# Kernel tuning notes

Measured on AMD Instinct MI355X. Metric: run time of the kernel, lower is better.

Reference implementation:

```python
import jax, jax.numpy as jnp
import numpy as np

LN_EPS = 1e-12


def setup_inputs() -> dict:
    key = jax.random.key(0)
    ks = jax.random.split(key, 5)
    b, t, n, di, do, de = 2, 3, 4096, 64, 64, 64
    return {
        "x": jax.random.normal(ks[0], (b, t, n, di), dtype=jnp.float32),
        "node_emb": jax.random.normal(ks[1], (n, de), dtype=jnp.float32),
        "time_emb": jax.random.normal(ks[2], (b, t, de), dtype=jnp.float32),
        "weights_pool": jax.random.normal(ks[3], (de, 2, di, do), dtype=jnp.float32) * 0.05,
        "bias_pool": jax.random.normal(ks[4], (de, do), dtype=jnp.float32) * 0.05,
        "ln_gamma": jnp.ones((de,), dtype=jnp.float32),
        "ln_beta": jnp.zeros((de,), dtype=jnp.float32),
    }


def reference(x, node_emb, time_emb, weights_pool, bias_pool, ln_gamma, ln_beta):
    # x: (b,t,n,di); node_emb: (n,de); time_emb: (b,t,de)
    # Dropout is identity in eval mode.
    e = node_emb[None, None, :, :] + time_emb[:, :, None, :]          # (b,t,n,de)
    mu = jnp.mean(e, axis=-1, keepdims=True)
    var = jnp.var(e, axis=-1, keepdims=True)
    e = (e - mu) * jax.lax.rsqrt(var + LN_EPS) * ln_gamma + ln_beta    # LayerNorm
    # Dynamic adjacency: softmax over source nodes
    supports2 = jax.nn.softmax(jnp.einsum("btnd,btmd->btnm", e, e), axis=-1)
    # supports1 is the identity matrix -> x_g1 == x
    x_g1 = x
    x_g2 = jnp.einsum("btnm,btmc->btnc", supports2, x)
    x_g = jnp.stack([x_g1, x_g2], axis=3)                              # (b,t,n,k=2,di)
    # Hypernetwork weights: node embeddings are identical for every t,
    # so tnd,dkio->tnkio reduces to nd,dkio->nkio (broadcast over t).
    weights = jnp.einsum("nd,dkio->nkio", node_emb, weights_pool)      # (n,2,di,do)
    bias = jnp.einsum("btd,do->bto", time_emb, bias_pool)              # (b,t,do)
    out = jnp.einsum("btnki,nkio->btno", x_g, weights) + bias[:, :, None, :]
    return out
```

## Files before the change

kernel.cpp:

```cpp
#include <hip/hip_runtime.h>


using bf16x8 = __attribute__((ext_vector_type(8))) __bf16;
using f32x4  = __attribute__((ext_vector_type(4))) float;
using f32x16 = __attribute__((ext_vector_type(16))) float;
using u32x4  = __attribute__((ext_vector_type(4))) unsigned int;

__device__ __forceinline__ unsigned short f2bf_bits(float f) {
    unsigned int u = __float_as_uint(f);
    u += 0x7fffu + ((u >> 16) & 1u);
    return (unsigned short)(u >> 16);
}

__device__ __forceinline__ unsigned int PK(float a, float b) {
    return __builtin_amdgcn_perm(__float_as_uint(b), __float_as_uint(a),
                                 0x07060302u);
}

__device__ __forceinline__ f32x4 mfma16(bf16x8 a, bf16x8 b, f32x4 c) {
    return __builtin_amdgcn_mfma_f32_16x16x32_bf16(a, b, c, 0, 0, 0);
}
__device__ __forceinline__ f32x16 mfma32(bf16x8 a, bf16x8 b, f32x16 c) {
    return __builtin_amdgcn_mfma_f32_32x32x16_bf16(a, b, c, 0, 0, 0);
}
__device__ __forceinline__ f32x16 zero16() {
    f32x16 z;
    #pragma unroll
    for (int i = 0; i < 16; ++i) z[i] = 0.f;
    return z;
}

__global__ __launch_bounds__(256) void k_prep(const float* __restrict__ x,
                                              const float* __restrict__ node_emb,
                                              const float* __restrict__ time_emb,
                                              const float* __restrict__ wp,
                                              const float* __restrict__ bias_pool,
                                              const float* __restrict__ gamma,
                                              const float* __restrict__ beta,
                                              unsigned short* __restrict__ eT,
                                              unsigned short* __restrict__ vT,
                                              unsigned short* __restrict__ ne_bf,
                                              unsigned short* __restrict__ wpB,
                                              float* __restrict__ biasw) {
    __shared__ float tile[64 * 65];
    const int b = blockIdx.x;
    const int t = threadIdx.x;
    if (b < 1536) {
        int lane = t & 63;
        int row0 = b * 16 + ((t >> 6) << 2);
        float gm = gamma[lane], bb2 = beta[lane];
        #pragma unroll
        for (int ri = 0; ri < 4; ++ri) {
            int rowf = row0 + ri;
            int bt = rowf >> 12, row = rowf & 4095;
            float v = node_emb[(row << 6) | lane] + time_emb[(bt << 6) | lane];
            float s = v, s2 = v * v;
            #pragma unroll
            for (int off = 32; off; off >>= 1) {
                s  += __shfl_xor(s,  off);
                s2 += __shfl_xor(s2, off);
            }
            float mu  = s * 0.015625f;
            float var = s2 * 0.015625f - mu * mu;
            float r   = rsqrtf(var + 1e-12f);
            float o   = (v - mu) * r * gm + bb2;
            size_t idx = (size_t)bt * 262144 + ((row >> 5) << 11)
                       + ((lane >> 4) << 9) + (((lane >> 3) & 1) << 8)
                       + ((row & 31) << 3) + (lane & 7);
            eT[idx] = f2bf_bits(o);
        }
    } else if (b < 1920) {
        int bb = b - 1536;
        int bt = bb >> 6, n0 = (bb & 63) << 6;
        const float* xr = x + ((size_t)((bt << 12) | n0) << 6);
        #pragma unroll
        for (int it = 0; it < 16; ++it) {
            int i = (it << 2) + (t >> 6);
            int d = t & 63;
            tile[i * 65 + d] = xr[(i << 6) + d];
        }
        __syncthreads();
        unsigned short* dst = vT + (size_t)bt * 262144;
        #pragma unroll
        for (int it = 0; it < 16; ++it) {
            int d = (it << 2) + (t >> 6);
            int n = t & 63;
            dst[(((n0 + n) >> 3) << 9) + (d << 3) + (n & 7)]
                = f2bf_bits(tile[n * 65 + d]);
        }
    } else if (b < 2944) {
        int idx = (b - 1920) * 256 + t;
        ne_bf[idx] = f2bf_bits(node_emb[idx]);
    } else if (b < 3072) {
        int ki = b - 2944;
        #pragma unroll
        for (int it = 0; it < 16; ++it) {
            int d = (it << 2) + (t >> 6);
            int o = t & 63;
            tile[d * 65 + o] = wp[(d << 13) + (ki << 6) + o];
        }
        __syncthreads();
        unsigned short* dst = wpB + ((size_t)ki << 12);
        #pragma unroll
        for (int it = 0; it < 2; ++it) {
            int u    = (it << 8) + t;
            int ot   = u >> 7;
            int frag = (u >> 6) & 1;
            int pos  = u & 63;
            int quad = pos >> 4, l16 = pos & 15;
            unsigned short* dp = dst + ((((ot << 1) + frag) << 9) + (pos << 3));
            #pragma unroll
            for (int j = 0; j < 8; ++j)
                dp[j] = f2bf_bits(
                    tile[((frag << 5) + (quad << 3) + j) * 65 + (ot << 4) + l16]);
        }
    } else {
        for (int idx = t; idx < 384; idx += 256) {
            int bt = idx >> 6, o = idx & 63;
            float bsum = 0.f;
            for (int d = 0; d < 64; ++d)
                bsum += time_emb[(bt << 6) + d] * bias_pool[(d << 6) + o];
            biasw[idx] = bsum;
        }
    }
}

__global__ __launch_bounds__(256, 3) void k_attn(const unsigned short* __restrict__ eT,
                                                 const unsigned short* __restrict__ vT,
                                                 float* __restrict__ P0,
                                                 float* __restrict__ P1,
                                                 float* __restrict__ L0,
                                                 float* __restrict__ L1) {
    __shared__ __align__(16) float Obuf[2][32 * 68];
    __shared__ float l_s[4][32];
    const int tid  = threadIdx.x;
    const int w    = tid >> 6;
    const int lane = tid & 63;
    const int l32  = lane & 31;
    const int h    = lane >> 5;

    const int bid   = blockIdx.x;
    const int half  = bid & 1;
    const int inner = bid >> 1;
    const int x8    = inner & 7;
    const int g     = (inner >> 3) & 31;
    const int r3    = inner >> 8;
    const int combo = x8 * 3 + r3;
    const int bt    = combo >> 2;
    const int qbase = ((((combo & 3) << 5) + g) << 5);

    const unsigned short* eb = eT + (size_t)bt * 262144;
    const unsigned short* vb = vT + (size_t)bt * 262144;
    float* Pout = half ? P1 : P0;
    float* Lout = half ? L1 : L0;

    const unsigned short* qp = eb + ((qbase >> 5) << 11) + (h << 8) + (l32 << 3);
    bf16x8 qf[4];
    #pragma unroll
    for (int c = 0; c < 4; ++c) {
        bf16x8 q = *(const bf16x8*)(qp + (c << 9));
        #pragma unroll
        for (int j = 0; j < 8; ++j) q[j] = (__bf16)((float)q[j] * 1.44269504f);
        qf[c] = q;
    }

    f32x16 O0 = zero16(), O1 = zero16();
    float lsa[4] = {0.f, 0.f, 0.f, 0.f};

    const int kstart = (half << 11) + (w << 9);
    const unsigned short* krBase = eb + ((kstart >> 5) << 11) + (h << 8) + (l32 << 3);
    const unsigned short* vrBase = vb + ((kstart >> 3) << 9) + (h << 9) + (l32 << 3);

    bf16x8 kA0, kA1, kA2, kA3, vA0, vA1, vA2, vA3;
    bf16x8 kB0, kB1, kB2, kB3, vB0, vB1, vB2, vB3;

#define LOAD_GRP(gi, K0, K1, K2, K3, V0, V1, V2, V3)                    \
    {                                                                   \
        const unsigned short* kp = krBase + ((gi) << 11);               \
        const unsigned short* vp = vrBase + ((gi) << 11);               \
        K0 = *(const bf16x8*)(kp);                                      \
        K1 = *(const bf16x8*)(kp + 512);                                \
        K2 = *(const bf16x8*)(kp + 1024);                               \
        K3 = *(const bf16x8*)(kp + 1536);                               \
        V0 = *(const bf16x8*)(vp);                                      \
        V1 = *(const bf16x8*)(vp + 256);                                \
        V2 = *(const bf16x8*)(vp + 1024);                               \
        V3 = *(const bf16x8*)(vp + 1280);                               \
    }

#define COMPUTE_GRP(K0, K1, K2, K3, V0, V1, V2, V3)                     \
    {                                                                   \
        f32x16 S = zero16();                                            \
        S = mfma32(K0, qf[0], S);                                       \
        S = mfma32(K1, qf[1], S);                                       \
        S = mfma32(K2, qf[2], S);                                       \
        S = mfma32(K3, qf[3], S);                                       \
        float p[16];                                                    \
        _Pragma("unroll")                                               \
        for (int r = 0; r < 16; ++r) p[r] = __builtin_amdgcn_exp2f(S[r]); \
        _Pragma("unroll")                                               \
        for (int r = 0; r < 4; ++r)                                     \
            lsa[r] += (p[r] + p[r + 4]) + (p[r + 8] + p[r + 12]);       \
        unsigned int Pa = PK(p[0], p[1]),   Pb = PK(p[2], p[3]);        \
        unsigned int Pc = PK(p[4], p[5]),   Pd = PK(p[6], p[7]);        \
        unsigned int Pe = PK(p[8], p[9]),   Pf = PK(p[10], p[11]);      \
        unsigned int Pg = PK(p[12], p[13]), Ph = PK(p[14], p[15]);      \
        unsigned int e0 = (unsigned int)__shfl_xor((int)(h ? Pa : Pc), 32); \
        unsigned int e1 = (unsigned int)__shfl_xor((int)(h ? Pb : Pd), 32); \
        unsigned int e2 = (unsigned int)__shfl_xor((int)(h ? Pe : Pg), 32); \
        unsigned int e3 = (unsigned int)__shfl_xor((int)(h ? Pf : Ph), 32); \
        u32x4 w0 = { h ? e0 : Pa, h ? e1 : Pb,                          \
                     h ? Pc : e0, h ? Pd : e1 };                        \
        u32x4 w1 = { h ? e2 : Pe, h ? e3 : Pf,                          \
                     h ? Pg : e2, h ? Ph : e3 };                        \
        bf16x8 pf0 = __builtin_bit_cast(bf16x8, w0);                    \
        bf16x8 pf1 = __builtin_bit_cast(bf16x8, w1);                    \
        O0 = mfma32(pf0, V0, O0);                                       \
        O1 = mfma32(pf0, V1, O1);                                       \
        O0 = mfma32(pf1, V2, O0);                                       \
        O1 = mfma32(pf1, V3, O1);                                       \
    }

    LOAD_GRP(0, kA0, kA1, kA2, kA3, vA0, vA1, vA2, vA3);
    for (int gi = 0; gi < 14; gi += 2) {
        LOAD_GRP(gi + 1, kB0, kB1, kB2, kB3, vB0, vB1, vB2, vB3);
        COMPUTE_GRP(kA0, kA1, kA2, kA3, vA0, vA1, vA2, vA3);
        LOAD_GRP(gi + 2, kA0, kA1, kA2, kA3, vA0, vA1, vA2, vA3);
        COMPUTE_GRP(kB0, kB1, kB2, kB3, vB0, vB1, vB2, vB3);
    }
    LOAD_GRP(15, kB0, kB1, kB2, kB3, vB0, vB1, vB2, vB3);
    COMPUTE_GRP(kA0, kA1, kA2, kA3, vA0, vA1, vA2, vA3);
    COMPUTE_GRP(kB0, kB1, kB2, kB3, vB0, vB1, vB2, vB3);
#undef LOAD_GRP
#undef COMPUTE_GRP

    float ls = (lsa[0] + lsa[1]) + (lsa[2] + lsa[3]);
    float lsum2 = ls + __shfl_xor(ls, 32);
    if (h == 0) l_s[w][l32] = lsum2;
    float* buf = Obuf[w & 1];
    if (w < 2) {
        #pragma unroll
        for (int r = 0; r < 16; ++r) {
            int qrow = (r & 3) + ((r >> 2) << 3) + (h << 2);
            buf[qrow * 68 + l32]      = O0[r];
            buf[qrow * 68 + 32 + l32] = O1[r];
        }
    }
    __syncthreads();
    if (w >= 2) {
        #pragma unroll
        for (int r = 0; r < 16; ++r) {
            int qrow = (r & 3) + ((r >> 2) << 3) + (h << 2);
            buf[qrow * 68 + l32]      += O0[r];
            buf[qrow * 68 + 32 + l32] += O1[r];
        }
    }
    __syncthreads();
    {
        int q  = tid >> 3;
        int d0 = (tid & 7) << 3;
        const float* b0 = Obuf[0] + q * 68 + d0;
        const float* b1 = Obuf[1] + q * 68 + d0;
        float* dst = Pout + (((size_t)(bt << 12) + qbase + q) << 6) + d0;
        #pragma unroll
        for (int i = 0; i < 8; ++i) dst[i] = b0[i] + b1[i];
        if ((tid & 7) == 0)
            Lout[(bt << 12) + qbase + q] =
                l_s[0][q] + l_s[1][q] + l_s[2][q] + l_s[3][q];
    }
}

__global__ __launch_bounds__(256, 2) void k_hyper(const float* __restrict__ x,
                                                  const float* __restrict__ P0,
                                                  const float* __restrict__ P1,
                                                  const float* __restrict__ L0,
                                                  const float* __restrict__ L1,
                                                  const unsigned short* __restrict__ ne_bf,
                                                  const unsigned short* __restrict__ wpB,
                                                  const float* __restrict__ bias_ws,
                                                  float* __restrict__ out) {
    __shared__ float smem[13056];
    __shared__ float invl_s[96];
    const int t    = threadIdx.x;
    const int w    = t >> 6;
    const int lane = t & 63;
    const int l16  = lane & 15;
    const int quad = lane >> 4;
    const int n0   = (blockIdx.x >> 1) << 4;
    const int oh   = blockIdx.x & 1;

    if (t < 96) {
        int bt = t % 6, nl = t / 6;
        int idx = (bt << 12) + n0 + nl;
        invl_s[t] = 1.f / (L0[idx] + L1[idx]);
    }
    __syncthreads();

    float* xg_s = smem + w * 3104;
    const int i0 = (w & 1) << 5;
    for (int it = 0; it < 48; ++it) {
        int j  = (it << 6) + lane;
        int kk = j & 31;
        int btnl = j >> 5;
        int bt = btnl % 6;
        int nl = btnl / 6;
        size_t idx = (((size_t)(bt << 12) + n0 + nl) << 6) + i0 + kk;
        float v;
        if (w < 2) v = x[idx];
        else       v = (P0[idx] + P1[idx]) * invl_s[btnl];
        xg_s[kk * 97 + btnl] = v;
    }
    __syncthreads();

    const unsigned short* nb = ne_bf + ((n0 + l16) << 6) + (quad << 3);
    bf16x8 a0 = *(const bf16x8*)(nb);
    bf16x8 a1 = *(const bf16x8*)(nb + 32);

    float oac[2][4][6];
    #pragma unroll
    for (int oc = 0; oc < 2; ++oc)
        #pragma unroll
        for (int r = 0; r < 4; ++r)
            #pragma unroll
            for (int bt = 0; bt < 6; ++bt) oac[oc][r][bt] = 0.f;

    const int ki_base = w << 5;
    #pragma unroll 2
    for (int kk = 0; kk < 32; ++kk) {
        const int ki = ki_base + kk;
        float g[4][6];
        #pragma unroll
        for (int r = 0; r < 4; ++r) {
            const float* gp = xg_s + kk * 97 + ((quad << 2) + r) * 6;
            #pragma unroll
            for (int bt = 0; bt < 6; ++bt) g[r][bt] = gp[bt];
        }
        #pragma unroll
        for (int oc = 0; oc < 2; ++oc) {
            const unsigned short* bp =
                wpB + ((((size_t)ki << 2) + (oh * 2 + oc)) << 10) + (lane << 3);
            bf16x8 b0 = *(const bf16x8*)(bp);
            bf16x8 b1 = *(const bf16x8*)(bp + 512);
            f32x4 wf = mfma16(a0, b0, f32x4{0.f, 0.f, 0.f, 0.f});
            wf = mfma16(a1, b1, wf);
            #pragma unroll
            for (int r = 0; r < 4; ++r)
                #pragma unroll
                for (int bt = 0; bt < 6; ++bt)
                    oac[oc][r][bt] += wf[r] * g[r][bt];
        }
    }

    __syncthreads();
    #pragma unroll
    for (int oc = 0; oc < 2; ++oc)
        #pragma unroll
        for (int r = 0; r < 4; ++r)
            #pragma unroll
            for (int bt = 0; bt < 6; ++bt)
                smem[w * 3264 + ((quad << 2) + r) * 204 + bt * 34 + (oc << 4) + l16]
                    = oac[oc][r][bt];
    __syncthreads();
    #pragma unroll
    for (int rr = 0; rr < 4; ++rr) {
        int nl = (w << 2) + rr;
        #pragma unroll
        for (int bp2 = 0; bp2 < 3; ++bp2) {
            int bt = bp2 * 2 + (lane >> 5);
            int ol = lane & 31;
            int o  = (oh << 5) + ol;
            int a  = nl * 204 + bt * 34 + ol;
            float v = smem[a] + smem[a + 3264] + smem[a + 6528] + smem[a + 9792]
                    + bias_ws[(bt << 6) + o];
            out[(((size_t)(bt << 12) + n0 + nl) << 6) + o] = v;
        }
    }
}

extern "C" void kernel_launch(void* const* d_in, const int* in_sizes, int n_in,
                              void* d_out, int out_size, void* d_ws, size_t ws_size,
                              hipStream_t stream) {
    const float* x         = (const float*)d_in[0];
    const float* node_emb  = (const float*)d_in[1];
    const float* time_emb  = (const float*)d_in[2];
    const float* wp        = (const float*)d_in[3];
    const float* bias_pool = (const float*)d_in[4];
    const float* gamma     = (const float*)d_in[5];
    const float* beta      = (const float*)d_in[6];
    float* out = (float*)d_out;

    char* wsb = (char*)d_ws;
    unsigned short* eT    = (unsigned short*)(wsb);
    unsigned short* vT    = (unsigned short*)(wsb + 3145728);
    float*          P0    = (float*)         (wsb + 6291456);
    float*          P1    = (float*)         (wsb + 12582912);
    unsigned short* wpB   = (unsigned short*)(wsb + 18874368);
    unsigned short* ne_bf = (unsigned short*)(wsb + 19922944);
    float*          biasw = (float*)         (wsb + 20447232);
    float*          L0    = (float*)         (wsb + 20448768);
    float*          L1    = (float*)         (wsb + 20547072);

    k_prep<<<3073, 256, 0, stream>>>(x, node_emb, time_emb, wp, bias_pool,
                                     gamma, beta, eT, vT, ne_bf, wpB, biasw);
    k_attn<<<1536, 256, 0, stream>>>(eT, vT, P0, P1, L0, L1);
    k_hyper<<<512, 256, 0, stream>>>(x, P0, P1, L0, L1, ne_bf, wpB, biasw, out);
}
```

Baseline: 143.9 us.

## Process 64 query rows per attention block to reuse K/V loads

Each attention block now handles two 32-row query tiles against the same loaded K and V fragments, so global K/V traffic per query is halved. The grid shrinks from 1536 to 768 blocks and the block-to-work mapping is changed to interleave across 8 groups, likely for XCD-aware scheduling. Per-thread register use roughly doubles for the accumulators and the launch bound drops to two blocks per CU, which lowers occupancy and the number of blocks available to hide latency.

```diff
diff --git a/kernel.cpp b/kernel.cpp
--- a/kernel.cpp
+++ b/kernel.cpp
@@ -125,29 +125,27 @@
     }
 }
 
-__global__ __launch_bounds__(256, 3) void k_attn(const unsigned short* __restrict__ eT,
+__global__ __launch_bounds__(256, 2) void k_attn(const unsigned short* __restrict__ eT,
                                                  const unsigned short* __restrict__ vT,
                                                  float* __restrict__ P0,
                                                  float* __restrict__ P1,
                                                  float* __restrict__ L0,
                                                  float* __restrict__ L1) {
-    __shared__ __align__(16) float Obuf[2][32 * 68];
-    __shared__ float l_s[4][32];
+    __shared__ __align__(16) float Obuf[2][64 * 68];
+    __shared__ float l_s[4][64];
     const int tid  = threadIdx.x;
     const int w    = tid >> 6;
     const int lane = tid & 63;
     const int l32  = lane & 31;
     const int h    = lane >> 5;
 
-    const int bid   = blockIdx.x;
-    const int half  = bid & 1;
-    const int inner = bid >> 1;
-    const int x8    = inner & 7;
-    const int g     = (inner >> 3) & 31;
-    const int r3    = inner >> 8;
-    const int combo = x8 * 3 + r3;
-    const int bt    = combo >> 2;
-    const int qbase = ((((combo & 3) << 5) + g) << 5);
+    const int bid     = (int)blockIdx.x;
+    const int logical = (bid & 7) * 96 + (bid >> 3);
+    const int set     = logical >> 6;
+    const int qc      = logical & 63;
+    const int bt      = set >> 1;
+    const int half    = set & 1;
+    const int qbase   = qc << 6;
 
     const unsigned short* eb = eT + (size_t)bt * 262144;
     const unsigned short* vb = vT + (size_t)bt * 262144;
@@ -155,17 +153,24 @@
     float* Lout = half ? L1 : L0;
 
     const unsigned short* qp = eb + ((qbase >> 5) << 11) + (h << 8) + (l32 << 3);
-    bf16x8 qf[4];
+    bf16x8 qf0[4], qf1[4];
     #pragma unroll
     for (int c = 0; c < 4; ++c) {
-        bf16x8 q = *(const bf16x8*)(qp + (c << 9));
-        #pragma unroll
-        for (int j = 0; j < 8; ++j) q[j] = (__bf16)((float)q[j] * 1.44269504f);
-        qf[c] = q;
-    }
-
-    f32x16 O0 = zero16(), O1 = zero16();
-    float lsa[4] = {0.f, 0.f, 0.f, 0.f};
+        bf16x8 q0 = *(const bf16x8*)(qp + (c << 9));
+        bf16x8 q1 = *(const bf16x8*)(qp + 2048 + (c << 9));
+        #pragma unroll
+        for (int j = 0; j < 8; ++j) {
+            q0[j] = (__bf16)((float)q0[j] * 1.44269504f);
+            q1[j] = (__bf16)((float)q1[j] * 1.44269504f);
+        }
+        qf0[c] = q0;
+        qf1[c] = q1;
+    }
+
+    f32x16 O00 = zero16(), O01 = zero16();
+    f32x16 O10 = zero16(), O11 = zero16();
+    float lsa0[4] = {0.f, 0.f, 0.f, 0.f};
+    float lsa1[4] = {0.f, 0.f, 0.f, 0.f};
 
     const int kstart = (half << 11) + (w << 9);
     const unsigned short* krBase = eb + ((kstart >> 5) << 11) + (h << 8) + (l32 << 3);
@@ -188,19 +193,19 @@
         V3 = *(const bf16x8*)(vp + 1280);                               \
     }
 
-#define COMPUTE_GRP(K0, K1, K2, K3, V0, V1, V2, V3)                     \
+#define QSET(QF, LSA, OA, OB, K0, K1, K2, K3, V0, V1, V2, V3)           \
     {                                                                   \
         f32x16 S = zero16();                                            \
-        S = mfma32(K0, qf[0], S);                                       \
-        S = mfma32(K1, qf[1], S);                                       \
-        S = mfma32(K2, qf[2], S);                                       \
-        S = mfma32(K3, qf[3], S);                                       \
+        S = mfma32(K0, QF[0], S);                                       \
+        S = mfma32(K1, QF[1], S);                                       \
+        S = mfma32(K2, QF[2], S);                                       \
+        S = mfma32(K3, QF[3], S);                                       \
         float p[16];                                                    \
         _Pragma("unroll")                                               \
         for (int r = 0; r < 16; ++r) p[r] = __builtin_amdgcn_exp2f(S[r]); \
         _Pragma("unroll")                                               \
         for (int r = 0; r < 4; ++r)                                     \
-            lsa[r] += (p[r] + p[r + 4]) + (p[r + 8] + p[r + 12]);       \
+            LSA[r] += (p[r] + p[r + 4]) + (p[r + 8] + p[r + 12]);       \
         unsigned int Pa = PK(p[0], p[1]),   Pb = PK(p[2], p[3]);        \
         unsigned int Pc = PK(p[4], p[5]),   Pd = PK(p[6], p[7]);        \
         unsigned int Pe = PK(p[8], p[9]),   Pf = PK(p[10], p[11]);      \
@@ -215,11 +220,15 @@
                      h ? Pg : e2, h ? Ph : e3 };                        \
         bf16x8 pf0 = __builtin_bit_cast(bf16x8, w0);                    \
         bf16x8 pf1 = __builtin_bit_cast(bf16x8, w1);                    \
-        O0 = mfma32(pf0, V0, O0);                                       \
-        O1 = mfma32(pf0, V1, O1);                                       \
-        O0 = mfma32(pf1, V2, O0);                                       \
-        O1 = mfma32(pf1, V3, O1);                                       \
-    }
+        OA = mfma32(pf0, V0, OA);                                       \
+        OB = mfma32(pf0, V1, OB);                                       \
+        OA = mfma32(pf1, V2, OA);                                       \
+        OB = mfma32(pf1, V3, OB);                                       \
+    }
+
+#define COMPUTE_GRP(K0, K1, K2, K3, V0, V1, V2, V3)                     \
+    QSET(qf0, lsa0, O00, O01, K0, K1, K2, K3, V0, V1, V2, V3)           \
+    QSET(qf1, lsa1, O10, O11, K0, K1, K2, K3, V0, V1, V2, V3)
 
     LOAD_GRP(0, kA0, kA1, kA2, kA3, vA0, vA1, vA2, vA3);
     for (int gi = 0; gi < 14; gi += 2) {
@@ -232,18 +241,26 @@
     COMPUTE_GRP(kA0, kA1, kA2, kA3, vA0, vA1, vA2, vA3);
     COMPUTE_GRP(kB0, kB1, kB2, kB3, vB0, vB1, vB2, vB3);
 #undef LOAD_GRP
+#undef QSET
 #undef COMPUTE_GRP
 
-    float ls = (lsa[0] + lsa[1]) + (lsa[2] + lsa[3]);
-    float lsum2 = ls + __shfl_xor(ls, 32);
-    if (h == 0) l_s[w][l32] = lsum2;
+    float ls0 = (lsa0[0] + lsa0[1]) + (lsa0[2] + lsa0[3]);
+    float ls1 = (lsa1[0] + lsa1[1]) + (lsa1[2] + lsa1[3]);
+    float l2_0 = ls0 + __shfl_xor(ls0, 32);
+    float l2_1 = ls1 + __shfl_xor(ls1, 32);
+    if (h == 0) {
+        l_s[w][l32]      = l2_0;
+        l_s[w][l32 + 32] = l2_1;
+    }
     float* buf = Obuf[w & 1];
     if (w < 2) {
         #pragma unroll
         for (int r = 0; r < 16; ++r) {
             int qrow = (r & 3) + ((r >> 2) << 3) + (h << 2);
-            buf[qrow * 68 + l32]      = O0[r];
-            buf[qrow * 68 + 32 + l32] = O1[r];
+            buf[qrow * 68 + l32]             = O00[r];
+            buf[qrow * 68 + 32 + l32]        = O01[r];
+            buf[(qrow + 32) * 68 + l32]      = O10[r];
+            buf[(qrow + 32) * 68 + 32 + l32] = O11[r];
         }
     }
     __syncthreads();
@@ -251,22 +268,28 @@
         #pragma unroll
         for (int r = 0; r < 16; ++r) {
             int qrow = (r & 3) + ((r >> 2) << 3) + (h << 2);
-            buf[qrow * 68 + l32]      += O0[r];
-            buf[qrow * 68 + 32 + l32] += O1[r];
+            buf[qrow * 68 + l32]             += O00[r];
+            buf[qrow * 68 + 32 + l32]        += O01[r];
+            buf[(qrow + 32) * 68 + l32]      += O10[r];
+            buf[(qrow + 32) * 68 + 32 + l32] += O11[r];
         }
     }
     __syncthreads();
     {
-        int q  = tid >> 3;
+        int q0 = tid >> 3;
         int d0 = (tid & 7) << 3;
-        const float* b0 = Obuf[0] + q * 68 + d0;
-        const float* b1 = Obuf[1] + q * 68 + d0;
-        float* dst = Pout + (((size_t)(bt << 12) + qbase + q) << 6) + d0;
-        #pragma unroll
-        for (int i = 0; i < 8; ++i) dst[i] = b0[i] + b1[i];
-        if ((tid & 7) == 0)
-            Lout[(bt << 12) + qbase + q] =
-                l_s[0][q] + l_s[1][q] + l_s[2][q] + l_s[3][q];
+        #pragma unroll
+        for (int qh = 0; qh < 2; ++qh) {
+            int q = q0 + (qh << 5);
+            const float* b0 = Obuf[0] + q * 68 + d0;
+            const float* b1 = Obuf[1] + q * 68 + d0;
+            float* dst = Pout + (((size_t)(bt << 12) + qbase + q) << 6) + d0;
+            #pragma unroll
+            for (int i = 0; i < 8; ++i) dst[i] = b0[i] + b1[i];
+            if ((tid & 7) == 0)
+                Lout[(bt << 12) + qbase + q] =
+                    l_s[0][q] + l_s[1][q] + l_s[2][q] + l_s[3][q];
+        }
     }
 }
 
@@ -402,6 +425,6 @@
 
     k_prep<<<3073, 256, 0, stream>>>(x, node_emb, time_emb, wp, bias_pool,
                                      gamma, beta, eT, vT, ne_bf, wpB, biasw);
-    k_attn<<<1536, 256, 0, stream>>>(eT, vT, P0, P1, L0, L1);
+    k_attn<<<768, 256, 0, stream>>>(eT, vT, P0, P1, L0, L1);
     k_hyper<<<512, 256, 0, stream>>>(x, P0, P1, L0, L1, ne_bf, wpB, biasw, out);
 }
```

New measurement: 139.8 us. 2.8% less time.
